# Performance work log

Measured on AMD Instinct MI355X. Metric: run time of the kernel, lower is better.

Reference implementation:

```python
import jax, jax.numpy as jnp
import numpy as np
from jax import lax

NEG = -1e30   # finite stand-in for -inf (keeps grads nan-free)
BLANK = 0


def _ctc_neg_log_lik(logprobs, labels, ilens, olens):
    """Per-sample CTC -log p(labels | logprobs).

    logprobs: [T, B, V] log-softmaxed frame posteriors
    labels:   [B, L] int padded targets (blank=0 never a real label)
    ilens:    [B] input lengths, olens: [B] label lengths
    """
    T, B, V = logprobs.shape
    L = labels.shape[1]
    S = 2 * L + 1
    s = jnp.arange(S)
    lab_idx = jnp.clip((s - 1) // 2, 0, L - 1)
    # extended label sequence: blank, y1, blank, y2, ..., blank  -> [B, S]
    ext = jnp.where((s % 2) == 1, labels[:, lab_idx], BLANK)
    prev2 = jnp.pad(ext[:, :-2], ((0, 0), (2, 0)), constant_values=BLANK)
    allow_skip = (s >= 2) & (ext != BLANK) & (ext != prev2)  # [B, S]

    # per-time log-probs of extended labels: [T, B, S]
    lp_ext = jnp.take_along_axis(
        logprobs, jnp.broadcast_to(ext[None], (T, B, S)), axis=2)

    def step(alpha, lp_t):
        a1 = alpha
        a2 = jnp.pad(alpha[:, :-1], ((0, 0), (1, 0)), constant_values=NEG)
        a3 = jnp.where(
            allow_skip,
            jnp.pad(alpha[:, :-2], ((0, 0), (2, 0)), constant_values=NEG),
            NEG)
        m = jnp.maximum(jnp.maximum(a1, a2), a3)
        new = m + jnp.log(jnp.exp(a1 - m) + jnp.exp(a2 - m) + jnp.exp(a3 - m)) + lp_t
        return new, new

    # alpha_{-1}: mass at s=0 only; first scan step then yields the standard
    # alpha_0[0]=lp0[blank], alpha_0[1]=lp0[y1], rest = -inf
    alpha0 = jnp.full((B, S), NEG, dtype=logprobs.dtype).at[:, 0].set(0.0)
    _, alphas = lax.scan(step, alpha0, lp_ext)  # [T, B, S]

    b_idx = jnp.arange(B)
    a_end = alphas[ilens - 1, b_idx]            # [B, S] alpha at last valid frame
    v1 = a_end[b_idx, 2 * olens]                # final blank
    v2 = a_end[b_idx, 2 * olens - 1]            # final label
    m = jnp.maximum(v1, v2)
    return -(m + jnp.log(jnp.exp(v1 - m) + jnp.exp(v2 - m)))  # [B]


def setup_inputs() -> dict:
    key = jax.random.key(0)
    k1, k2, k3, k4, k5 = jax.random.split(key, 5)
    B, T, D, V, L = 16, 800, 512, 5000, 100
    hs_pad = jax.random.normal(k1, (B, T, D), dtype=jnp.float32)
    hlens = jax.random.randint(k2, (B,), 700, T + 1, dtype=jnp.int32)
    ys_pad = jax.random.randint(k3, (B, L), 1, V, dtype=jnp.int32)
    ys_lens = jax.random.randint(k4, (B,), 50, L + 1, dtype=jnp.int32)
    W = jax.random.normal(k5, (V, D), dtype=jnp.float32) * (1.0 / np.sqrt(D))
    b = jnp.zeros((V,), dtype=jnp.float32)
    return {"hs_pad": hs_pad, "hlens": hlens, "ys_pad": ys_pad,
            "ys_lens": ys_lens, "W": W, "b": b}


def reference(hs_pad, hlens, ys_pad, ys_lens, W, b):
    B = hs_pad.shape[0]
    # ctc_lo linear (dropout p=0 is identity)
    logits = jnp.einsum('btd,vd->btv', hs_pad, W) + b        # [B, T, V]
    lp = jax.nn.log_softmax(logits, axis=-1)
    lp = jnp.transpose(lp, (1, 0, 2))                         # [T, B, V]
    loss = _ctc_neg_log_lik(lp, ys_pad, hlens, ys_lens)       # [B]
    # reduce=True: loss.sum() / size (size == B; all samples finite)
    return loss.sum() / B
```

## Files before the change

### kernel.cpp

```cpp
#include <hip/hip_runtime.h>
#include <stdint.h>

#define NEG (-1e30f)
#define LOG2E 1.4426950408889634f
#define LN2 0.6931471805599453f
#define NS 5
#define CPB 32

typedef __attribute__((ext_vector_type(8))) short bf16x8;
typedef __attribute__((ext_vector_type(4))) float f32x4;

__device__ __forceinline__ unsigned short f2bf(float f) {
  unsigned u = __builtin_bit_cast(unsigned, f);
  unsigned r = u + 0x7FFFu + ((u >> 16) & 1u);
  return (unsigned short)(r >> 16);
}
__device__ __forceinline__ float exp2_fast(float x) {
  float r; asm("v_exp_f32 %0, %1" : "=v"(r) : "v"(x)); return r;
}
__device__ __forceinline__ float log2_fast(float x) {
  float r; asm("v_log_f32 %0, %1" : "=v"(r) : "v"(x)); return r;
}
__device__ __forceinline__ float ldexp_fast(float x, int n) {
  float r; asm("v_ldexp_f32 %0, %1, %2" : "=v"(r) : "v"(x), "v"(n)); return r;
}
__device__ __forceinline__ float dpp_shr1(float x) {
  int r = __builtin_amdgcn_update_dpp(0, __builtin_bit_cast(int, x),
                                      0x138, 0xf, 0xf, false);
  return __builtin_bit_cast(float, r);
}
__device__ __forceinline__ float dpp_shr1_keep(float x) {
  int xi = __builtin_bit_cast(int, x);
  int r = __builtin_amdgcn_update_dpp(xi, xi, 0x138, 0xf, 0xf, false);
  return __builtin_bit_cast(float, r);
}

__global__ void cvt_h_kernel(const float* __restrict__ src,
                             unsigned short* __restrict__ dst, int n4) {
  int i = blockIdx.x * 256 + threadIdx.x;
  if (i >= n4) return;
  float4 v = ((const float4*)src)[i];
  ushort4 o;
  o.x = f2bf(v.x); o.y = f2bf(v.y); o.z = f2bf(v.z); o.w = f2bf(v.w);
  ((ushort4*)dst)[i] = o;
}

__global__ void cvt_w_kernel(const float* __restrict__ W,
                             unsigned short* __restrict__ dst,
                             int V, int D4, int n4) {
  int i = blockIdx.x * 256 + threadIdx.x;
  if (i >= n4) return;
  int row = i / D4;
  ushort4 o = {0, 0, 0, 0};
  if (row < V) {
    float4 v = ((const float4*)W)[i];
    o.x = f2bf(v.x); o.y = f2bf(v.y); o.z = f2bf(v.z); o.w = f2bf(v.w);
  }
  ((ushort4*)dst)[i] = o;
}

__device__ __forceinline__ void stage32(const unsigned short* Wbf, unsigned char* sbuf,
                                        float* sb, const float* bias, int c, int V, int tid) {
  const unsigned char* base = (const unsigned char*)Wbf + ((size_t)c << 15);
#pragma unroll
  for (int i = 0; i < 8; ++i) {
    int dest = (i << 12) + (tid << 4);
    int row = dest >> 10;
    int src = (row << 10) + ((dest & 1023) ^ ((row & 15) << 4));
    __builtin_amdgcn_global_load_lds(
        (const __attribute__((address_space(1))) unsigned int*)(base + src),
        (__attribute__((address_space(3))) unsigned int*)(sbuf + dest), 16, 0, 0);
  }
  if (tid < 32) {
    int vg = (c << 5) + tid;
    sb[tid] = (vg < V) ? bias[vg] : 0.f;
  }
}

__launch_bounds__(256, 2)
__global__ void lse_kernel(const unsigned short* __restrict__ Hbf,
                           const unsigned short* __restrict__ Wbf,
                           const float* __restrict__ bias,
                           float2* __restrict__ lse_p,
                           int V, int NC_tot, int M) {
  __shared__ __align__(16) unsigned char sW[2][32768];
  __shared__ float sbias[2][32];
  const int tid = threadIdx.x;
  const int lane = tid & 63;
  const int w = tid >> 6;
  const int vl = lane & 15, kq = lane >> 4;
  const int mblk = blockIdx.x % 100;
  const int split = blockIdx.x / 100;
  const int c0 = split * CPB;
  const int c1 = min(NC_tot, c0 + CPB);
  const int rowbase = mblk * 128 + w * 32;

  bf16x8 bq0[16], bq1[16];
  {
    const unsigned short* h0 = Hbf + (size_t)(rowbase + vl) * 512 + kq * 8;
    const unsigned short* h1 = Hbf + (size_t)(rowbase + 16 + vl) * 512 + kq * 8;
#pragma unroll
    for (int ks = 0; ks < 16; ++ks) {
      bq0[ks] = *(const bf16x8*)(h0 + ks * 32);
      bq1[ks] = *(const bf16x8*)(h1 + ks * 32);
    }
  }

  stage32(Wbf, sW[0], sbias[0], bias, c0, V, tid);
  int cur = 0;
  float mx0 = NEG, sm0 = 0.f, mx1 = NEG, sm1 = 0.f;

  for (int c = c0; c < c1; ++c) {
    asm volatile("s_waitcnt vmcnt(0)" ::: "memory");
    __syncthreads();
    if (c + 1 < c1) stage32(Wbf, sW[cur ^ 1], sbias[cur ^ 1], bias, c + 1, V, tid);

    f32x4 a00 = 0.f, a01 = 0.f, a10 = 0.f, a11 = 0.f;
#pragma unroll
    for (int ks = 0; ks < 16; ++ks) {
      int inrow = (ks * 64 + kq * 16) ^ (vl << 4);
      bf16x8 A0 = *(const bf16x8*)(&sW[cur][(vl << 10) + inrow]);
      bf16x8 A1 = *(const bf16x8*)(&sW[cur][16384 + (vl << 10) + inrow]);
      a00 = __builtin_amdgcn_mfma_f32_16x16x32_bf16(A0, bq0[ks], a00, 0, 0, 0);
      a01 = __builtin_amdgcn_mfma_f32_16x16x32_bf16(A0, bq1[ks], a01, 0, 0, 0);
      a10 = __builtin_amdgcn_mfma_f32_16x16x32_bf16(A1, bq0[ks], a10, 0, 0, 0);
      a11 = __builtin_amdgcn_mfma_f32_16x16x32_bf16(A1, bq1[ks], a11, 0, 0, 0);
    }
    float lg0[8], lg1[8];
#pragma unroll
    for (int g = 0; g < 2; ++g)
#pragma unroll
      for (int j = 0; j < 4; ++j) {
        int vloc = g * 16 + kq * 4 + j;
        bool ok = (c * 32 + vloc) < V;
        float bb = sbias[cur][vloc];
        float x0 = (g == 0) ? a00[j] : a10[j];
        float x1 = (g == 0) ? a01[j] : a11[j];
        lg0[g * 4 + j] = ok ? (x0 + bb) : NEG;
        lg1[g * 4 + j] = ok ? (x1 + bb) : NEG;
      }
    float lm0 = lg0[0], lm1 = lg1[0];
#pragma unroll
    for (int i = 1; i < 8; ++i) { lm0 = fmaxf(lm0, lg0[i]); lm1 = fmaxf(lm1, lg1[i]); }
    float nm0 = fmaxf(mx0, lm0), nm1 = fmaxf(mx1, lm1);
    float s0 = 0.f, s1 = 0.f;
#pragma unroll
    for (int i = 0; i < 8; ++i) { s0 += __expf(lg0[i] - nm0); s1 += __expf(lg1[i] - nm1); }
    sm0 = sm0 * __expf(mx0 - nm0) + s0;  mx0 = nm0;
    sm1 = sm1 * __expf(mx1 - nm1) + s1;  mx1 = nm1;
    cur ^= 1;
  }

#pragma unroll
  for (int d = 16; d <= 32; d <<= 1) {
    float omx = __shfl_xor(mx0, d), osm = __shfl_xor(sm0, d);
    float nm = fmaxf(mx0, omx);
    sm0 = sm0 * __expf(mx0 - nm) + osm * __expf(omx - nm); mx0 = nm;
    omx = __shfl_xor(mx1, d); osm = __shfl_xor(sm1, d);
    nm = fmaxf(mx1, omx);
    sm1 = sm1 * __expf(mx1 - nm) + osm * __expf(omx - nm); mx1 = nm;
  }
  if (lane < 16) {
    lse_p[(size_t)split * M + rowbase + vl]      = make_float2(mx0, sm0);
    lse_p[(size_t)split * M + rowbase + 16 + vl] = make_float2(mx1, sm1);
  }
}

__global__ void lse_merge(const float2* __restrict__ lse_p, float* __restrict__ lse, int M) {
  int i = blockIdx.x * 256 + threadIdx.x;
  if (i >= M) return;
  float mx = NEG, sm = 0.f;
#pragma unroll
  for (int s = 0; s < NS; ++s) {
    float2 p = lse_p[(size_t)s * M + i];
    float nm = fmaxf(mx, p.x);
    sm = sm * __expf(mx - nm) + p.y * __expf(p.x - nm);
    mx = nm;
  }
  lse[i] = mx + __logf(sm);
}

__launch_bounds__(256, 1)
__global__ void sel_kernel(const unsigned short* __restrict__ Hbf,
                           const unsigned short* __restrict__ Wbf,
                           const float* __restrict__ bias,
                           const int* __restrict__ ys,
                           const float* __restrict__ lse,
                           float* __restrict__ lp,
                           int B, int T, int L) {
  __shared__ __align__(16) unsigned char sWs[114688];
  __shared__ float sb[112];
  const int tid = threadIdx.x, lane = tid & 63, w = tid >> 6;
  const int vl = lane & 15, kq = lane >> 4;
  const int b = blockIdx.x / 7;
  const int mt = blockIdx.x % 7;

  int vocs[28];
#pragma unroll
  for (int i = 0; i < 28; ++i) {
    int n = w * 28 + i;
    vocs[i] = (n < L) ? ys[b * L + n] : 0;
  }
#pragma unroll
  for (int i = 0; i < 28; ++i) {
    int n = w * 28 + i;
    const unsigned char* src = (const unsigned char*)Wbf + ((size_t)vocs[i] << 10);
    int soff = (lane << 4) ^ ((n & 15) << 4);
    __builtin_amdgcn_global_load_lds(
        (const __attribute__((address_space(1))) unsigned int*)(src + soff),
        (__attribute__((address_space(3))) unsigned int*)(sWs + (n << 10) + (lane << 4)), 16, 0, 0);
  }
  if (tid < 112) {
    int voc = (tid < L) ? ys[b * L + tid] : 0;
    sb[tid] = bias[voc];
  }

  const int trow0 = mt * 128 + w * 32;
  bf16x8 bq0[16], bq1[16];
  {
    int t0 = min(trow0 + vl, T - 1), t1 = min(trow0 + 16 + vl, T - 1);
    const unsigned short* h0 = Hbf + (size_t)(b * T + t0) * 512 + kq * 8;
    const unsigned short* h1 = Hbf + (size_t)(b * T + t1) * 512 + kq * 8;
#pragma unroll
    for (int ks = 0; ks < 16; ++ks) {
      bq0[ks] = *(const bf16x8*)(h0 + ks * 32);
      bq1[ks] = *(const bf16x8*)(h1 + ks * 32);
    }
  }
  float ls0 = lse[b * T + min(trow0 + vl, T - 1)];
  float ls1 = lse[b * T + min(trow0 + 16 + vl, T - 1)];

  asm volatile("s_waitcnt vmcnt(0)" ::: "memory");
  __syncthreads();

  f32x4 acc[7][2];
#pragma unroll
  for (int g = 0; g < 7; ++g) { acc[g][0] = 0.f; acc[g][1] = 0.f; }
#pragma unroll
  for (int ks = 0; ks < 16; ++ks) {
    int inrow = (ks * 64 + kq * 16) ^ (vl << 4);
#pragma unroll
    for (int g = 0; g < 7; ++g) {
      bf16x8 A = *(const bf16x8*)(&sWs[((g * 16 + vl) << 10) + inrow]);
      acc[g][0] = __builtin_amdgcn_mfma_f32_16x16x32_bf16(A, bq0[ks], acc[g][0], 0, 0, 0);
      acc[g][1] = __builtin_amdgcn_mfma_f32_16x16x32_bf16(A, bq1[ks], acc[g][1], 0, 0, 0);
    }
  }

  float bv0, bv1;
  {
    float m0 = acc[6][0][0] + sb[100];
    float m1 = acc[6][1][0] + sb[100];
    bv0 = __shfl(m0, 16 + vl, 64);
    bv1 = __shfl(m1, 16 + vl, 64);
  }

#pragma unroll
  for (int rs = 0; rs < 2; ++rs) {
    int trow = trow0 + rs * 16 + vl;
    if (trow >= T) continue;
    float ls = rs ? ls1 : ls0;
    float bv = rs ? bv1 : bv0;
    float* orow = lp + (size_t)(b * T + trow) * 112;
#pragma unroll
    for (int g = 0; g < 7; ++g) {
      int n0 = g * 16 + kq * 4;
      if (n0 < 100) {
        float4 o;
        o.x = exp2_fast((acc[g][rs][0] + sb[n0 + 0] - bv) * LOG2E);
        o.y = exp2_fast((acc[g][rs][1] + sb[n0 + 1] - bv) * LOG2E);
        o.z = exp2_fast((acc[g][rs][2] + sb[n0 + 2] - bv) * LOG2E);
        o.w = exp2_fast((acc[g][rs][3] + sb[n0 + 3] - bv) * LOG2E);
        *(float4*)(orow + n0) = o;
      } else if (n0 == 100) {
        float4 o = {(bv - ls) * LOG2E, 0.f, 0.f, 0.f};
        *(float4*)(orow + n0) = o;
      }
    }
  }
}


#define PH_ISSUE(P, Bk, tb_)                                              \
  _Pragma("unroll") for (int i = 0; i < 16; ++i) {                        \
    int tt = (tb_) + i; tt = (tt < ilen) ? tt : (ilen - 1);               \
    const float* r = lpb + (size_t)tt * 112;                              \
    asm volatile("global_load_dwordx2 %0, %1, off"                        \
                 : "=v"(P[i]) : "v"(r + pidx));                           \
    asm volatile("global_load_dword %0, %1, off"                          \
                 : "=v"(Bk[i]) : "v"(r + L));                             \
  }                                                                       \
  __builtin_amdgcn_sched_barrier(0);

#define DP_STEP(px_, py_, cb_)                                            \
  {                                                                       \
    float pm1 = dpp_shr1(A3);                                             \
    pm1 = ldexp_fast(pm1, dneg);                                          \
    float u1 = A0 + A1; u1 = fmaf(pm1, msk1, u1);                         \
    float u3 = A2 + A3; u3 = fmaf(A1, msk3, u3);                          \
    A0 = A0 + pm1;                                                        \
    A2 = A1 + A2;                                                         \
    A1 = u1 * (px_);                                                      \
    A3 = u3 * (py_);                                                      \
    cbs += (cb_);                                                         \
  }

#define DP_STEP_M(px_, py_, cb_, act)                                     \
  {                                                                       \
    float pm1 = dpp_shr1(A3);                                             \
    pm1 = ldexp_fast(pm1, dneg);                                          \
    float u1 = A0 + A1; u1 = fmaf(pm1, msk1, u1);                         \
    float u3 = A2 + A3; u3 = fmaf(A1, msk3, u3);                          \
    float t0 = A0 + pm1;                                                  \
    float t2 = A1 + A2;                                                   \
    float t1 = u1 * (px_);                                                \
    float t3 = u3 * (py_);                                                \
    if (act) { A0 = t0; A1 = t1; A2 = t2; A3 = t3; cbs += (cb_); }        \
  }

#define RESCALE                                                           \
  {                                                                       \
    float m_ = fmaxf(fmaxf(A0, A1), fmaxf(A2, A3));                       \
    int u_ = __builtin_bit_cast(int, m_);                                 \
    int e_ = u_ >> 23;                                                    \
    bool nz_ = (u_ != 0);                                                 \
    float sc_ = nz_ ? __builtin_bit_cast(float, (254 - e_) << 23) : 1.f;  \
    A0 *= sc_; A1 *= sc_; A2 *= sc_; A3 *= sc_;                           \
    lsc += nz_ ? (float)(e_ - 127) : 0.f;                                 \
    float lp_ = dpp_shr1_keep(lsc);                                       \
    lsc = nz_ ? lsc : lp_;                                                \
    int d_ = (int)(lp_ - lsc);                                            \
    dneg = d_ > 126 ? 126 : d_;                                           \
  }

#define PH_COMP(P, Bk)                                                    \
  _Pragma("unroll") for (int i = 0; i < 16; ++i) {                        \
    DP_STEP(P[i].x, P[i].y, Bk[i])                                        \
    if ((i & 3) == 3) RESCALE                                             \
  }

#define PH_COMP_M(P, Bk, tb_)                                             \
  _Pragma("unroll") for (int i = 0; i < 16; ++i) {                        \
    DP_STEP_M(P[i].x, P[i].y, Bk[i], ((tb_) + i) < ilen)                  \
    if ((i & 3) == 3) RESCALE                                             \
  }

__launch_bounds__(64)
__global__ void ctc_dp_kernel(const float* __restrict__ lp, const int* __restrict__ ys,
                              const int* __restrict__ hlens, const int* __restrict__ olens,
                              float* __restrict__ loss, int T, int L) {
  __shared__ float arr[256];
  __shared__ float lscarr[64];
  const int b = blockIdx.x;
  const int lane = threadIdx.x;
  const int ilen = hlens[b];
  const int Smax = 2 * L;

  float msk1, msk3;
  {
    int s1 = 4 * lane + 1, s3 = 4 * lane + 3;
    int i1 = min((s1 - 1) >> 1, L - 1), i1p = max(0, min((s1 - 3) >> 1, L - 1));
    int i3 = min((s3 - 1) >> 1, L - 1), i3p = max(0, min((s3 - 3) >> 1, L - 1));
    int lab1 = ys[b * L + i1], lab1p = ys[b * L + i1p];
    int lab3 = ys[b * L + i3], lab3p = ys[b * L + i3p];
    msk1 = ((s1 <= Smax) && (s1 >= 3) && (lab1 != lab1p)) ? 1.f : 0.f;
    msk3 = ((s3 <= Smax) && (s3 >= 3) && (lab3 != lab3p)) ? 1.f : 0.f;
  }
  const int lim = (Smax - 3) >> 2;
  const int pidx = (lane <= lim) ? 2 * lane : (L + 2);

  const float* lpb = lp + (size_t)(b * T) * 112;

  float A0 = (lane == 0) ? 1.f : 0.f, A1 = 0.f, A2 = 0.f, A3 = 0.f;
  float lsc = 0.f, cbs = 0.f;
  int dneg = 0;

  float2 pA[16], pB[16], pC[16];
  float bA[16], bB[16], bC[16];
  const int nph = (ilen + 15) >> 4;

  PH_ISSUE(pA, bA, 0)
  PH_ISSUE(pB, bB, 16)
  for (int k = 0; k < nph; ++k) {
    const int tb = k << 4;
    asm volatile("s_waitcnt vmcnt(32)" ::: "memory");
    __builtin_amdgcn_sched_barrier(0);
    const int m3 = k - (k / 3) * 3;
    const bool lastm = (k == nph - 1);
    if (m3 == 0) {
      PH_ISSUE(pC, bC, tb + 32)
      if (lastm) { PH_COMP_M(pA, bA, tb) } else { PH_COMP(pA, bA) }
    } else if (m3 == 1) {
      PH_ISSUE(pA, bA, tb + 32)
      if (lastm) { PH_COMP_M(pB, bB, tb) } else { PH_COMP(pB, bB) }
    } else {
      PH_ISSUE(pB, bB, tb + 32)
      if (lastm) { PH_COMP_M(pC, bC, tb) } else { PH_COMP(pC, bC) }
    }
  }
  asm volatile("s_waitcnt vmcnt(0)" ::: "memory");
  __builtin_amdgcn_sched_barrier(0);

  arr[lane * 4 + 0] = A0; arr[lane * 4 + 1] = A1;
  arr[lane * 4 + 2] = A2; arr[lane * 4 + 3] = A3;
  lscarr[lane] = lsc;
  __syncthreads();
  if (lane == 0) {
    int ol = olens[b];
    float aN = arr[2 * ol], aNm = arr[2 * ol - 1];
    float l1 = lscarr[(2 * ol) >> 2], l2 = lscarr[(2 * ol - 1) >> 2];
    float mm = fmaxf(l1, l2);
    float v = ldexp_fast(aN, (int)(l1 - mm)) + ldexp_fast(aNm, (int)(l2 - mm));
    loss[b] = -LN2 * (log2_fast(v) + mm + cbs);
  }
}

__global__ void finalize_kernel(const float* __restrict__ loss, float* __restrict__ out, int B) {
  float v = ((int)threadIdx.x < B) ? loss[threadIdx.x] : 0.f;
#pragma unroll
  for (int m = 1; m <= 32; m <<= 1) v += __shfl_xor(v, m);
  if (threadIdx.x == 0) out[0] = v / (float)B;
}

extern "C" void kernel_launch(void* const* d_in, const int* in_sizes, int n_in,
                              void* d_out, int out_size, void* d_ws, size_t ws_size,
                              hipStream_t stream) {
  const float* hs    = (const float*)d_in[0];
  const int*   hlens = (const int*)d_in[1];
  const int*   ys    = (const int*)d_in[2];
  const int*   olens = (const int*)d_in[3];
  const float* W     = (const float*)d_in[4];
  const float* bias  = (const float*)d_in[5];

  int B = in_sizes[1];
  int L = in_sizes[2] / B;
  int V = in_sizes[5];
  int D = in_sizes[4] / V;
  int T = in_sizes[0] / (B * D);
  int Vp = (V + 63) & ~63;
  int M = B * T;
  int NC_tot = Vp / 32;

  char* ws = (char*)d_ws;
  unsigned short* Hbf = (unsigned short*)ws;
  size_t off = (size_t)M * D * 2;
  unsigned short* Wbf = (unsigned short*)(ws + off);
  off += (size_t)Vp * D * 2;
  float* lse = (float*)(ws + off);
  off += (size_t)M * 4;
  off = (off + 255) & ~(size_t)255;
  float2* lse_p = (float2*)(ws + off);
  off += (size_t)NS * M * 8;
  off = (off + 255) & ~(size_t)255;
  float* lp = (float*)(ws + off);
  off += (size_t)M * 112 * 4;
  float* loss = (float*)(ws + off);

  int n4h = M * D / 4;
  cvt_h_kernel<<<(n4h + 255) / 256, 256, 0, stream>>>(hs, Hbf, n4h);
  int n4w = Vp * D / 4;
  cvt_w_kernel<<<(n4w + 255) / 256, 256, 0, stream>>>(W, Wbf, V, D / 4, n4w);
  lse_kernel<<<100 * NS, 256, 0, stream>>>(Hbf, Wbf, bias, lse_p, V, NC_tot, M);
  lse_merge<<<(M + 255) / 256, 256, 0, stream>>>(lse_p, lse, M);
  sel_kernel<<<B * 7, 256, 0, stream>>>(Hbf, Wbf, bias, ys, lse, lp, B, T, L);
  ctc_dp_kernel<<<B, 64, 0, stream>>>(lp, ys, hlens, olens, loss, T, L);
  finalize_kernel<<<1, 64, 0, stream>>>(loss, (float*)d_out, B);
}
```

Before: 162.0 us.

## Process two CTC samples per wavefront with interleaved DP chains

The CTC alpha recursion now runs two batch samples in one 64-lane block, interleaving their independent dependency chains so each hides the other's latency. The prefetch pipeline drops from three 16-step asm-issued buffers to two 8-step buffers loaded with plain C++. The separate per-step blank-scale load is removed: lane lim+1 reads the blank column through its normal float2 load, its label factor is masked to zero, and its accumulated sum is fetched with readlane at the end. This halves the block count, so fewer CUs work on the DP, and removes the explicit vmcnt control over memory latency.

```diff
diff --git a/kernel.cpp b/kernel.cpp
--- a/kernel.cpp
+++ b/kernel.cpp
@@ -280,45 +280,46 @@
   }
 }
 
-
-#define PH_ISSUE(P, Bk, tb_)                                              \
-  _Pragma("unroll") for (int i = 0; i < 16; ++i) {                        \
-    int tt = (tb_) + i; tt = (tt < ilen) ? tt : (ilen - 1);               \
-    const float* r = lpb + (size_t)tt * 112;                              \
-    asm volatile("global_load_dwordx2 %0, %1, off"                        \
-                 : "=v"(P[i]) : "v"(r + pidx));                           \
-    asm volatile("global_load_dword %0, %1, off"                          \
-                 : "=v"(Bk[i]) : "v"(r + L));                             \
-  }                                                                       \
-  __builtin_amdgcn_sched_barrier(0);
-
-#define DP_STEP(px_, py_, cb_)                                            \
+#define DEPTH 8
+
+#define LOADP(PX, PY, tb_)                                                \
+  _Pragma("unroll") for (int i = 0; i < DEPTH; ++i) {                     \
+    int tt = (tb_) + i;                                                   \
+    int tx = (tt < ilenX) ? tt : (ilenX - 1);                             \
+    int ty = (tt < ilenY) ? tt : (ilenY - 1);                             \
+    PX[i] = *(const float2*)(lpbX + (size_t)tx * 112 + pidx);             \
+    PY[i] = *(const float2*)(lpbY + (size_t)ty * 112 + pidx);             \
+  }
+
+#define DP1(A0, A1, A2, A3, m1_, m3_, dneg, cbs, PV)                      \
   {                                                                       \
     float pm1 = dpp_shr1(A3);                                             \
     pm1 = ldexp_fast(pm1, dneg);                                          \
-    float u1 = A0 + A1; u1 = fmaf(pm1, msk1, u1);                         \
-    float u3 = A2 + A3; u3 = fmaf(A1, msk3, u3);                          \
+    float px = (PV).x * vmx;                                              \
+    float u1 = A0 + A1; u1 = fmaf(pm1, m1_, u1);                          \
+    float u3 = A2 + A3; u3 = fmaf(A1, m3_, u3);                           \
     A0 = A0 + pm1;                                                        \
     A2 = A1 + A2;                                                         \
-    A1 = u1 * (px_);                                                      \
-    A3 = u3 * (py_);                                                      \
-    cbs += (cb_);                                                         \
-  }
-
-#define DP_STEP_M(px_, py_, cb_, act)                                     \
+    A1 = u1 * px;                                                         \
+    A3 = u3 * (PV).y;                                                     \
+    cbs += (PV).x;                                                        \
+  }
+
+#define DP1M(A0, A1, A2, A3, m1_, m3_, dneg, cbs, PV, act)                \
   {                                                                       \
     float pm1 = dpp_shr1(A3);                                             \
     pm1 = ldexp_fast(pm1, dneg);                                          \
-    float u1 = A0 + A1; u1 = fmaf(pm1, msk1, u1);                         \
-    float u3 = A2 + A3; u3 = fmaf(A1, msk3, u3);                          \
+    float px = (PV).x * vmx;                                              \
+    float u1 = A0 + A1; u1 = fmaf(pm1, m1_, u1);                          \
+    float u3 = A2 + A3; u3 = fmaf(A1, m3_, u3);                           \
     float t0 = A0 + pm1;                                                  \
     float t2 = A1 + A2;                                                   \
-    float t1 = u1 * (px_);                                                \
-    float t3 = u3 * (py_);                                                \
-    if (act) { A0 = t0; A1 = t1; A2 = t2; A3 = t3; cbs += (cb_); }        \
-  }
-
-#define RESCALE                                                           \
+    float t1 = u1 * px;                                                   \
+    float t3 = u3 * (PV).y;                                               \
+    if (act) { A0 = t0; A1 = t1; A2 = t2; A3 = t3; cbs += (PV).x; }       \
+  }
+
+#define RES1(A0, A1, A2, A3, lsc, dneg)                                   \
   {                                                                       \
     float m_ = fmaxf(fmaxf(A0, A1), fmaxf(A2, A3));                       \
     int u_ = __builtin_bit_cast(int, m_);                                 \
@@ -333,85 +334,106 @@
     dneg = d_ > 126 ? 126 : d_;                                           \
   }
 
-#define PH_COMP(P, Bk)                                                    \
-  _Pragma("unroll") for (int i = 0; i < 16; ++i) {                        \
-    DP_STEP(P[i].x, P[i].y, Bk[i])                                        \
-    if ((i & 3) == 3) RESCALE                                             \
-  }
-
-#define PH_COMP_M(P, Bk, tb_)                                             \
-  _Pragma("unroll") for (int i = 0; i < 16; ++i) {                        \
-    DP_STEP_M(P[i].x, P[i].y, Bk[i], ((tb_) + i) < ilen)                  \
-    if ((i & 3) == 3) RESCALE                                             \
+#define PH2(PX, PY)                                                       \
+  _Pragma("unroll") for (int i = 0; i < DEPTH; ++i) {                     \
+    DP1(X0, X1, X2, X3, mX1, mX3, dnegX, cbsX, PX[i])                     \
+    DP1(Y0, Y1, Y2, Y3, mY1, mY3, dnegY, cbsY, PY[i])                     \
+    if ((i & 3) == 3) {                                                   \
+      RES1(X0, X1, X2, X3, lscX, dnegX)                                   \
+      RES1(Y0, Y1, Y2, Y3, lscY, dnegY)                                   \
+    }                                                                     \
+  }
+
+#define PH2M(PX, PY, tb_)                                                 \
+  _Pragma("unroll") for (int i = 0; i < DEPTH; ++i) {                     \
+    bool aX = ((tb_) + i) < ilenX, aY = ((tb_) + i) < ilenY;              \
+    DP1M(X0, X1, X2, X3, mX1, mX3, dnegX, cbsX, PX[i], aX)                \
+    DP1M(Y0, Y1, Y2, Y3, mY1, mY3, dnegY, cbsY, PY[i], aY)                \
+    if ((i & 3) == 3) {                                                   \
+      RES1(X0, X1, X2, X3, lscX, dnegX)                                   \
+      RES1(Y0, Y1, Y2, Y3, lscY, dnegY)                                   \
+    }                                                                     \
   }
 
 __launch_bounds__(64)
 __global__ void ctc_dp_kernel(const float* __restrict__ lp, const int* __restrict__ ys,
                               const int* __restrict__ hlens, const int* __restrict__ olens,
                               float* __restrict__ loss, int T, int L) {
-  __shared__ float arr[256];
-  __shared__ float lscarr[64];
-  const int b = blockIdx.x;
+  __shared__ float arr[2][256];
+  __shared__ float lscarr[2][64];
+  const int b0 = blockIdx.x * 2;
   const int lane = threadIdx.x;
-  const int ilen = hlens[b];
+  const int ilenX = hlens[b0], ilenY = hlens[b0 + 1];
   const int Smax = 2 * L;
 
-  float msk1, msk3;
+  float mX1, mX3, mY1, mY3;
   {
     int s1 = 4 * lane + 1, s3 = 4 * lane + 3;
     int i1 = min((s1 - 1) >> 1, L - 1), i1p = max(0, min((s1 - 3) >> 1, L - 1));
     int i3 = min((s3 - 1) >> 1, L - 1), i3p = max(0, min((s3 - 3) >> 1, L - 1));
-    int lab1 = ys[b * L + i1], lab1p = ys[b * L + i1p];
-    int lab3 = ys[b * L + i3], lab3p = ys[b * L + i3p];
-    msk1 = ((s1 <= Smax) && (s1 >= 3) && (lab1 != lab1p)) ? 1.f : 0.f;
-    msk3 = ((s3 <= Smax) && (s3 >= 3) && (lab3 != lab3p)) ? 1.f : 0.f;
+    bool v1 = (s1 <= Smax) && (s1 >= 3), v3 = (s3 <= Smax) && (s3 >= 3);
+    int a = ys[b0 * L + i1], ap = ys[b0 * L + i1p];
+    int c = ys[b0 * L + i3], cp = ys[b0 * L + i3p];
+    mX1 = (v1 && (a != ap)) ? 1.f : 0.f;
+    mX3 = (v3 && (c != cp)) ? 1.f : 0.f;
+    a = ys[(b0 + 1) * L + i1]; ap = ys[(b0 + 1) * L + i1p];
+    c = ys[(b0 + 1) * L + i3]; cp = ys[(b0 + 1) * L + i3p];
+    mY1 = (v1 && (a != ap)) ? 1.f : 0.f;
+    mY3 = (v3 && (c != cp)) ? 1.f : 0.f;
   }
   const int lim = (Smax - 3) >> 2;
-  const int pidx = (lane <= lim) ? 2 * lane : (L + 2);
-
-  const float* lpb = lp + (size_t)(b * T) * 112;
-
-  float A0 = (lane == 0) ? 1.f : 0.f, A1 = 0.f, A2 = 0.f, A3 = 0.f;
-  float lsc = 0.f, cbs = 0.f;
-  int dneg = 0;
-
-  float2 pA[16], pB[16], pC[16];
-  float bA[16], bB[16], bC[16];
-  const int nph = (ilen + 15) >> 4;
-
-  PH_ISSUE(pA, bA, 0)
-  PH_ISSUE(pB, bB, 16)
+  const int pidx = (lane <= lim) ? 2 * lane : ((lane == lim + 1) ? L : (L + 2));
+  const float vmx = (lane == lim + 1) ? 0.f : 1.f;
+
+  const float* lpbX = lp + (size_t)(b0 * T) * 112;
+  const float* lpbY = lp + (size_t)((b0 + 1) * T) * 112;
+
+  float X0 = (lane == 0) ? 1.f : 0.f, X1 = 0.f, X2 = 0.f, X3 = 0.f;
+  float Y0 = (lane == 0) ? 1.f : 0.f, Y1 = 0.f, Y2 = 0.f, Y3 = 0.f;
+  float lscX = 0.f, cbsX = 0.f, lscY = 0.f, cbsY = 0.f;
+  int dnegX = 0, dnegY = 0;
+
+  float2 XA[DEPTH], XB[DEPTH], YA[DEPTH], YB[DEPTH];
+  const int maxI = max(ilenX, ilenY), minI = min(ilenX, ilenY);
+  const int nph = (maxI + DEPTH - 1) / DEPTH;
+
+  LOADP(XA, YA, 0)
+  __builtin_amdgcn_sched_barrier(0);
   for (int k = 0; k < nph; ++k) {
-    const int tb = k << 4;
-    asm volatile("s_waitcnt vmcnt(32)" ::: "memory");
+    const int tb = k * DEPTH;
+    const bool needM = (tb + DEPTH) > minI;
+    if (k & 1) {
+      if (k + 1 < nph) { LOADP(XA, YA, tb + DEPTH) }
+      __builtin_amdgcn_sched_barrier(0);
+      if (needM) { PH2M(XB, YB, tb) } else { PH2(XB, YB) }
+    } else {
+      if (k + 1 < nph) { LOADP(XB, YB, tb + DEPTH) }
+      __builtin_amdgcn_sched_barrier(0);
+      if (needM) { PH2M(XA, YA, tb) } else { PH2(XA, YA) }
+    }
     __builtin_amdgcn_sched_barrier(0);
-    const int m3 = k - (k / 3) * 3;
-    const bool lastm = (k == nph - 1);
-    if (m3 == 0) {
-      PH_ISSUE(pC, bC, tb + 32)
-      if (lastm) { PH_COMP_M(pA, bA, tb) } else { PH_COMP(pA, bA) }
-    } else if (m3 == 1) {
-      PH_ISSUE(pA, bA, tb + 32)
-      if (lastm) { PH_COMP_M(pB, bB, tb) } else { PH_COMP(pB, bB) }
-    } else {
-      PH_ISSUE(pB, bB, tb + 32)
-      if (lastm) { PH_COMP_M(pC, bC, tb) } else { PH_COMP(pC, bC) }
-    }
-  }
-  asm volatile("s_waitcnt vmcnt(0)" ::: "memory");
-  __builtin_amdgcn_sched_barrier(0);
-
-  arr[lane * 4 + 0] = A0; arr[lane * 4 + 1] = A1;
-  arr[lane * 4 + 2] = A2; arr[lane * 4 + 3] = A3;
-  lscarr[lane] = lsc;
+  }
+
+  arr[0][lane * 4 + 0] = X0; arr[0][lane * 4 + 1] = X1;
+  arr[0][lane * 4 + 2] = X2; arr[0][lane * 4 + 3] = X3;
+  arr[1][lane * 4 + 0] = Y0; arr[1][lane * 4 + 1] = Y1;
+  arr[1][lane * 4 + 2] = Y2; arr[1][lane * 4 + 3] = Y3;
+  lscarr[0][lane] = lscX; lscarr[1][lane] = lscY;
+  float cb0 = __builtin_bit_cast(float,
+      __builtin_amdgcn_readlane(__builtin_bit_cast(int, cbsX), lim + 1));
+  float cb1 = __builtin_bit_cast(float,
+      __builtin_amdgcn_readlane(__builtin_bit_cast(int, cbsY), lim + 1));
   __syncthreads();
   if (lane == 0) {
-    int ol = olens[b];
-    float aN = arr[2 * ol], aNm = arr[2 * ol - 1];
-    float l1 = lscarr[(2 * ol) >> 2], l2 = lscarr[(2 * ol - 1) >> 2];
-    float mm = fmaxf(l1, l2);
-    float v = ldexp_fast(aN, (int)(l1 - mm)) + ldexp_fast(aNm, (int)(l2 - mm));
-    loss[b] = -LN2 * (log2_fast(v) + mm + cbs);
+#pragma unroll
+    for (int s = 0; s < 2; ++s) {
+      int ol = olens[b0 + s];
+      float aN = arr[s][2 * ol], aNm = arr[s][2 * ol - 1];
+      float l1 = lscarr[s][(2 * ol) >> 2], l2 = lscarr[s][(2 * ol - 1) >> 2];
+      float mm = fmaxf(l1, l2);
+      float v = ldexp_fast(aN, (int)(l1 - mm)) + ldexp_fast(aNm, (int)(l2 - mm));
+      loss[b0 + s] = -LN2 * (log2_fast(v) + mm + (s ? cb1 : cb0));
+    }
   }
 }
 
@@ -463,6 +485,6 @@
   lse_kernel<<<100 * NS, 256, 0, stream>>>(Hbf, Wbf, bias, lse_p, V, NC_tot, M);
   lse_merge<<<(M + 255) / 256, 256, 0, stream>>>(lse_p, lse, M);
   sel_kernel<<<B * 7, 256, 0, stream>>>(Hbf, Wbf, bias, ys, lse, lp, B, T, L);
-  ctc_dp_kernel<<<B, 64, 0, stream>>>(lp, ys, hlens, olens, loss, T, L);
+  ctc_dp_kernel<<<B / 2, 64, 0, stream>>>(lp, ys, hlens, olens, loss, T, L);
   finalize_kernel<<<1, 64, 0, stream>>>(loss, (float*)d_out, B);
 }
```

Result: slower. 199.7 us (+23.3%).
